# Optimization experiments

Measured on AMD Instinct MI355X. Metric: run time of the kernel, lower is better.

Reference implementation:

```python
import jax, jax.numpy as jnp
import numpy as np

EMB = 256
HEADS = 4
HEAD_DIM = EMB // HEADS
N = 4096
M = 4096


def setup_inputs() -> dict:
    key = jax.random.key(0)
    ks = jax.random.split(key, 7)
    s = 1.0 / np.sqrt(EMB)  # keep logits in a sane range
    return {
        "A": jax.random.normal(ks[0], (N, EMB), jnp.float32),
        "B": jax.random.normal(ks[1], (M, EMB), jnp.float32),
        "Wq": jax.random.normal(ks[2], (EMB, EMB), jnp.float32) * s,
        "Wk": jax.random.normal(ks[3], (EMB, EMB), jnp.float32) * s,
        "Wv": jax.random.normal(ks[4], (EMB, EMB), jnp.float32) * s,
        "Wo": jax.random.normal(ks[5], (EMB, EMB), jnp.float32) * s,
        "bo": jnp.zeros((EMB,), jnp.float32),
    }


def _cross_attend(X, Y, Wq, Wk, Wv, Wo, bo):
    # X attends to Y. X:[n,emb], Y:[m,emb]
    scale = jnp.asarray(np.sqrt(HEAD_DIM), X.dtype)
    Q = (X @ Wq.T).reshape(X.shape[0], HEADS, HEAD_DIM)  # [n,h,d]
    K = (Y @ Wk.T).reshape(Y.shape[0], HEADS, HEAD_DIM)  # [m,h,d]
    V = (Y @ Wv.T).reshape(Y.shape[0], HEADS, HEAD_DIM)  # [m,h,d]
    scores = jnp.einsum("nhd,mhd->hnm", Q, K) / scale      # [h,n,m]
    attn = jax.nn.softmax(scores, axis=-1)                   # dropout p=0.0 -> identity
    ctx = jnp.einsum("hnm,mhd->nhd", attn, V).reshape(X.shape[0], EMB)
    return ctx @ Wo.T + bo + X                               # out proj + residual


def reference(A, B, Wq, Wk, Wv, Wo, bo):
    A_out = _cross_attend(A, B, Wq, Wk, Wv, Wo, bo)
    B_out = _cross_attend(B, A, Wq, Wk, Wv, Wo, bo)
    return (A_out, B_out)
```

## Files before the change

### kernel.cpp

```cpp
#include <hip/hip_runtime.h>
#include <hip/hip_bf16.h>
#include <math.h>

#define EMB 256
#define HEADS 4
#define HD 64
#define NTOK 4096

typedef __attribute__((ext_vector_type(8))) short bf16x8;
typedef __attribute__((ext_vector_type(4))) float f32x4;
typedef __attribute__((ext_vector_type(16))) float f32x16;

#define MFMA16(a, b, c) __builtin_amdgcn_mfma_f32_16x16x32_bf16(a, b, c, 0, 0, 0)
#define MFMA32(a, b, c) __builtin_amdgcn_mfma_f32_32x32x16_bf16(a, b, c, 0, 0, 0)

static __device__ __forceinline__ ushort f2bf(float f) {
    __hip_bfloat16 h = __float2bfloat16(f);
    return *(ushort*)&h;
}
static __device__ __forceinline__ float ex2(float x) { return __builtin_amdgcn_exp2f(x); }
static __device__ __forceinline__ uint pkbf(float lo, float hi) {
    uint r;
    asm("v_cvt_pk_bf16_f32 %0, %1, %2" : "=v"(r) : "v"(lo), "v"(hi));
    return r;
}
static __device__ __forceinline__ float max3f(float a, float b, float c) {
    float r;
    asm("v_max3_f32 %0, %1, %2, %3" : "=v"(r) : "v"(a), "v"(b), "v"(c));
    return r;
}
static __device__ __forceinline__ bf16x8 cvt8(float4 a, float4 b) {
    union { uint u[4]; bf16x8 h; } pk;
    pk.u[0] = pkbf(a.x, a.y);
    pk.u[1] = pkbf(a.z, a.w);
    pk.u[2] = pkbf(b.x, b.y);
    pk.u[3] = pkbf(b.z, b.w);
    return pk.h;
}
static __device__ __forceinline__ float bf2f(ushort u) {
    return __uint_as_float(((uint)u) << 16);
}

__global__ void cvtW(const float* __restrict__ Wq, const float* __restrict__ Wk,
                     const float* __restrict__ Wv, const float* __restrict__ Wo,
                     ushort* __restrict__ Wall) {
    const float* s = (blockIdx.y == 0) ? Wq : (blockIdx.y == 1) ? Wk : (blockIdx.y == 2) ? Wv : Wo;
    ushort* d = Wall + (size_t)blockIdx.y * 65536;
    int i = (blockIdx.x * 256 + threadIdx.x) * 4;
    float4 v = *(const float4*)(s + i);
    ushort4 o;
    o.x = f2bf(v.x); o.y = f2bf(v.y); o.z = f2bf(v.z); o.w = f2bf(v.w);
    *(ushort4*)(d + i) = o;
}

__global__ __launch_bounds__(256) void qkv_proj(const float* __restrict__ Xa,
                                                const float* __restrict__ Xb,
                                                const ushort* __restrict__ Wall,
                                                ushort* __restrict__ Q0, ushort* __restrict__ K1, ushort* __restrict__ Vt1,
                                                ushort* __restrict__ Q1, ushort* __restrict__ K0, ushort* __restrict__ Vt0) {
    int w = threadIdx.x >> 6, lane = threadIdx.x & 63;
    int lr = lane & 15, lg = lane >> 4;
    int z = blockIdx.z;
    int kind = (z < 3) ? z : z - 3;
    const float* X = (z < 3) ? Xa : Xb;
    ushort* Qo = (z < 3) ? Q0 : Q1;
    ushort* Ko = (z < 3) ? K1 : K0;
    ushort* Vto = (z < 3) ? Vt1 : Vt0;
    const ushort* W = Wall + (size_t)kind * 65536;
    int rbase = blockIdx.x * 64 + w * 16;
    int cbase = blockIdx.y * 64;

    f32x4 acc[4] = {};
#pragma unroll
    for (int kk = 0; kk < 256; kk += 32) {
        const float* xr = X + (size_t)(rbase + lr) * EMB + kk + lg * 8;
        bf16x8 a = cvt8(*(const float4*)xr, *(const float4*)(xr + 4));
#pragma unroll
        for (int cj = 0; cj < 4; ++cj) {
            bf16x8 b = *(const bf16x8*)(W + (size_t)(cbase + cj * 16 + lr) * EMB + kk + lg * 8);
            acc[cj] = MFMA16(a, b, acc[cj]);
        }
    }
    const float QS = 0.125f * 1.4426950408889634f;
#pragma unroll
    for (int cj = 0; cj < 4; ++cj)
#pragma unroll
        for (int j = 0; j < 4; ++j) {
            int R = rbase + lg * 4 + j;
            int col = cbase + cj * 16 + lr;
            float v = acc[cj][j];
            if (kind == 0) {
                Qo[(size_t)R * EMB + col] = f2bf(v * QS);
            } else if (kind == 1) {
                Ko[(size_t)R * EMB + col] = f2bf(v);
            } else {
                int h = col >> 6, d = col & 63;
                int Rp = (R & ~12) | ((R & 4) << 1) | ((R & 8) >> 1);
                Vto[(size_t)h * HD * NTOK + (size_t)d * NTOK + Rp] = f2bf(v);
            }
        }
}

__global__ __launch_bounds__(256, 4) void attn(const ushort* __restrict__ Q0,
                                               const ushort* __restrict__ K0,
                                               const ushort* __restrict__ Vt0,
                                               const ushort* __restrict__ Q1,
                                               const ushort* __restrict__ K1,
                                               const ushort* __restrict__ Vt1,
                                               ushort* __restrict__ Opart,
                                               float* __restrict__ ML) {
    __shared__ ushort lK[2][64 * 64];
    __shared__ ushort lV[2][64 * 64];

    int fb = blockIdx.x + 32 * blockIdx.y + 128 * blockIdx.z;
    int nf = (fb & 7) * 128 + (fb >> 3);
    int qt = nf & 31;
    int head = (nf >> 5) & 3;
    int z = nf >> 7;
    int dir = z >> 2, split = z & 3;
    int kv0 = split * 1024;

    const ushort* Q = dir ? Q1 : Q0;
    const ushort* K = dir ? K1 : K0;
    const ushort* Vt = dir ? Vt1 : Vt0;
    const ushort* Vth = Vt + (size_t)head * HD * NTOK;

    int wq = threadIdx.x >> 6;
    int lane = threadIdx.x & 63;
    int l31 = lane & 31, hi = lane >> 5;

    int qg = qt * 128 + wq * 32 + l31;
    bf16x8 qf[4];
#pragma unroll
    for (int ks = 0; ks < 4; ++ks)
        qf[ks] = *(const bf16x8*)(Q + (size_t)qg * EMB + head * 64 + ks * 16 + hi * 8);

    int srow = threadIdx.x >> 3, sseg = threadIdx.x & 7;
    int ssw0 = (sseg ^ (srow & 7)) * 8;
    int ssw1 = (sseg ^ ((srow + 32) & 7)) * 8;

    uint4 rk0 = *(const uint4*)(K + (size_t)(kv0 + srow) * EMB + head * 64 + sseg * 8);
    uint4 rk1 = *(const uint4*)(K + (size_t)(kv0 + srow + 32) * EMB + head * 64 + sseg * 8);
    uint4 rv0 = *(const uint4*)(Vth + (size_t)srow * NTOK + kv0 + sseg * 8);
    uint4 rv1 = *(const uint4*)(Vth + (size_t)(srow + 32) * NTOK + kv0 + sseg * 8);

    float m = -1e30f, ls = 0.0f;
    f32x16 oacc0 = {};
    f32x16 oacc1 = {};
    int sw = l31 & 7;

    for (int t = 0; t < 16; ++t) {
        int cur = t & 1;
        ushort* lk = &lK[cur][0];
        ushort* lv = &lV[cur][0];
        *(uint4*)(&lk[srow * 64 + ssw0]) = rk0;
        *(uint4*)(&lk[(srow + 32) * 64 + ssw1]) = rk1;
        *(uint4*)(&lv[srow * 64 + ssw0]) = rv0;
        *(uint4*)(&lv[(srow + 32) * 64 + ssw1]) = rv1;
        __syncthreads();

        if (t < 15) {
            int nkv = kv0 + (t + 1) * 64;
            rk0 = *(const uint4*)(K + (size_t)(nkv + srow) * EMB + head * 64 + sseg * 8);
            rk1 = *(const uint4*)(K + (size_t)(nkv + srow + 32) * EMB + head * 64 + sseg * 8);
            rv0 = *(const uint4*)(Vth + (size_t)srow * NTOK + nkv + sseg * 8);
            rv1 = *(const uint4*)(Vth + (size_t)(srow + 32) * NTOK + nkv + sseg * 8);
        }

        f32x16 sA = {}, sB = {};
        __builtin_amdgcn_s_setprio(1);
#pragma unroll
        for (int ks = 0; ks < 4; ++ks) {
            bf16x8 ka = *(const bf16x8*)(&lk[l31 * 64 + ((ks * 2 + hi) ^ sw) * 8]);
            bf16x8 kb = *(const bf16x8*)(&lk[(32 + l31) * 64 + ((ks * 2 + hi) ^ sw) * 8]);
            sA = MFMA32(ka, qf[ks], sA);
            sB = MFMA32(kb, qf[ks], sB);
        }
        __builtin_amdgcn_s_setprio(0);

        float t0 = max3f(sA[0], sA[1], sA[2]);
        float t1 = max3f(sA[3], sA[4], sA[5]);
        float t2 = max3f(sA[6], sA[7], sA[8]);
        float t3 = max3f(sA[9], sA[10], sA[11]);
        float t4 = max3f(sA[12], sA[13], sA[14]);
        float t5 = max3f(sB[0], sB[1], sB[2]);
        float t6 = max3f(sB[3], sB[4], sB[5]);
        float t7 = max3f(sB[6], sB[7], sB[8]);
        float t8 = max3f(sB[9], sB[10], sB[11]);
        float t9 = max3f(sB[12], sB[13], sB[14]);
        float ta = fmaxf(sA[15], sB[15]);
        float u0 = max3f(t0, t1, t2);
        float u1 = max3f(t3, t4, t5);
        float u2 = max3f(t6, t7, t8);
        float u3 = fmaxf(t9, ta);
        float tmax = fmaxf(max3f(u0, u1, u2), u3);
        tmax = fmaxf(tmax, __shfl_xor(tmax, 32));

        if (__any(tmax > m + 8.0f)) {
            float mn = fmaxf(m, tmax);
            float sc = ex2(m - mn);
            m = mn;
            ls *= sc;
#pragma unroll
            for (int r = 0; r < 16; ++r) { oacc0[r] *= sc; oacc1[r] *= sc; }
        }

#pragma unroll
        for (int r = 0; r < 16; ++r) sA[r] = ex2(sA[r] - m);
#pragma unroll
        for (int r = 0; r < 16; ++r) sB[r] = ex2(sB[r] - m);

        float s1[16];
#pragma unroll
        for (int i = 0; i < 8; ++i) s1[i] = sA[2 * i] + sA[2 * i + 1];
#pragma unroll
        for (int i = 0; i < 8; ++i) s1[8 + i] = sB[2 * i] + sB[2 * i + 1];
#pragma unroll
        for (int w2 = 8; w2 >= 1; w2 >>= 1)
#pragma unroll
            for (int i = 0; i < 8; ++i)
                if (i < w2) s1[i] = s1[2 * i] + s1[2 * i + 1];
        float rs = s1[0];
        rs += __shfl_xor(rs, 32);
        ls += rs;

        bf16x8 pa[4];
#pragma unroll
        for (int ks = 0; ks < 4; ++ks) {
            union { uint u[4]; bf16x8 h; } pk;
#pragma unroll
            for (int j = 0; j < 4; ++j) {
                float lo = (ks < 2) ? sA[(ks & 1) * 8 + 2 * j] : sB[(ks & 1) * 8 + 2 * j];
                float hv = (ks < 2) ? sA[(ks & 1) * 8 + 2 * j + 1] : sB[(ks & 1) * 8 + 2 * j + 1];
                pk.u[j] = pkbf(lo, hv);
            }
            pa[ks] = pk.h;
        }

        __builtin_amdgcn_s_setprio(1);
#pragma unroll
        for (int ks = 0; ks < 4; ++ks) {
            bf16x8 va = *(const bf16x8*)(&lv[l31 * 64 + ((ks * 2 + hi) ^ sw) * 8]);
            bf16x8 vb = *(const bf16x8*)(&lv[(32 + l31) * 64 + ((ks * 2 + hi) ^ sw) * 8]);
            oacc0 = MFMA32(va, pa[ks], oacc0);
            oacc1 = MFMA32(vb, pa[ks], oacc1);
        }
        __builtin_amdgcn_s_setprio(0);
    }

    ushort* Ob = Opart + ((size_t)z * 4096 + qg) * 256 + head * 64;
#pragma unroll
    for (int r = 0; r < 16; ++r) {
        int crow = (r & 3) + 8 * (r >> 2) + 4 * hi;
        Ob[crow] = f2bf(oacc0[r]);
        Ob[32 + crow] = f2bf(oacc1[r]);
    }
    if (hi == 0) {
        float2* mlp = (float2*)ML;
        mlp[((size_t)z * 4 + head) * 4096 + qg] = make_float2(m, ls);
    }
}

__global__ __launch_bounds__(256) void out_proj(const ushort* __restrict__ Opart,
                                                const float* __restrict__ ML,
                                                const ushort* __restrict__ Wo,
                                                const float* __restrict__ bo,
                                                const float* __restrict__ A,
                                                const float* __restrict__ B,
                                                float* __restrict__ out) {
    int dir = blockIdx.z;
    const float* X = dir ? B : A;
    float* o = out + (size_t)dir * NTOK * EMB;

    int w = threadIdx.x >> 6, lane = threadIdx.x & 63;
    int lr = lane & 15, lg = lane >> 4;
    int rbase = blockIdx.x * 64 + w * 16;
    int cbase = blockIdx.y * 64;
    int R = rbase + lr;

    const float2* mlp = (const float2*)ML;
    float Wm[4][4];
#pragma unroll
    for (int h = 0; h < 4; ++h) {
        float2 ml[4];
        float M = -1e30f;
#pragma unroll
        for (int s = 0; s < 4; ++s) {
            ml[s] = mlp[((size_t)(dir * 4 + s) * 4 + h) * 4096 + R];
            M = fmaxf(M, ml[s].x);
        }
        float denom = 0.0f, a[4];
#pragma unroll
        for (int s = 0; s < 4; ++s) { a[s] = ex2(ml[s].x - M); denom += a[s] * ml[s].y; }
        float inv = 1.0f / denom;
#pragma unroll
        for (int s = 0; s < 4; ++s) Wm[h][s] = a[s] * inv;
    }

    const ushort* Or[4];
#pragma unroll
    for (int s = 0; s < 4; ++s)
        Or[s] = Opart + ((size_t)(dir * 4 + s) * 4096 + R) * 256;

    f32x4 acc[4] = {};
#pragma unroll
    for (int kk = 0; kk < 256; kk += 32) {
        int h = kk >> 6;
        bf16x8 xs0 = *(const bf16x8*)(Or[0] + kk + lg * 8);
        bf16x8 xs1 = *(const bf16x8*)(Or[1] + kk + lg * 8);
        bf16x8 xs2 = *(const bf16x8*)(Or[2] + kk + lg * 8);
        bf16x8 xs3 = *(const bf16x8*)(Or[3] + kk + lg * 8);
        float cv[8];
#pragma unroll
        for (int u = 0; u < 8; ++u) {
            cv[u] = Wm[h][0] * bf2f((ushort)xs0[u]) + Wm[h][1] * bf2f((ushort)xs1[u])
                  + Wm[h][2] * bf2f((ushort)xs2[u]) + Wm[h][3] * bf2f((ushort)xs3[u]);
        }
        float4 c0 = {cv[0], cv[1], cv[2], cv[3]};
        float4 c1 = {cv[4], cv[5], cv[6], cv[7]};
        bf16x8 a = cvt8(c0, c1);
#pragma unroll
        for (int cj = 0; cj < 4; ++cj) {
            bf16x8 b = *(const bf16x8*)(Wo + (size_t)(cbase + cj * 16 + lr) * EMB + kk + lg * 8);
            acc[cj] = MFMA16(a, b, acc[cj]);
        }
    }
#pragma unroll
    for (int cj = 0; cj < 4; ++cj)
#pragma unroll
        for (int j = 0; j < 4; ++j) {
            int Rr = rbase + lg * 4 + j;
            int col = cbase + cj * 16 + lr;
            o[(size_t)Rr * EMB + col] = acc[cj][j] + bo[col] + X[(size_t)Rr * EMB + col];
        }
}

extern "C" void kernel_launch(void* const* d_in, const int* in_sizes, int n_in,
                              void* d_out, int out_size, void* d_ws, size_t ws_size,
                              hipStream_t stream) {
    const float* A  = (const float*)d_in[0];
    const float* B  = (const float*)d_in[1];
    const float* Wq = (const float*)d_in[2];
    const float* Wk = (const float*)d_in[3];
    const float* Wv = (const float*)d_in[4];
    const float* Wo = (const float*)d_in[5];
    const float* bo = (const float*)d_in[6];
    float* out = (float*)d_out;

    ushort* ws = (ushort*)d_ws;
    const size_t TE = (size_t)NTOK * EMB;
    ushort* wall = ws;
    ushort* q0  = wall + 4 * 65536;
    ushort* q1  = q0 + TE;
    ushort* k0  = q1 + TE;
    ushort* k1  = k0 + TE;
    ushort* vt0 = k1 + TE;
    ushort* vt1 = vt0 + TE;
    ushort* Opart = vt1 + TE;
    float* ML = (float*)(Opart + (size_t)8 * 4096 * 256);

    cvtW<<<dim3(64, 4), 256, 0, stream>>>(Wq, Wk, Wv, Wo, wall);

    qkv_proj<<<dim3(64, 4, 6), 256, 0, stream>>>(A, B, wall, q0, k1, vt1, q1, k0, vt0);

    attn<<<dim3(32, 4, 8), 256, 0, stream>>>(q0, k0, vt0, q1, k1, vt1, Opart, ML);

    out_proj<<<dim3(64, 4, 2), 256, 0, stream>>>(Opart, ML, wall + 3 * 65536, bo, A, B, out);
}
```

Baseline: 113.8 us.

## Single-buffer K/V in LDS, change swizzle, use permlane32 swap for reductions

Result: no change. 113.4 us (-0.4%).

```diff
diff --git a/kernel.cpp b/kernel.cpp
--- a/kernel.cpp
+++ b/kernel.cpp
@@ -10,6 +10,7 @@
 typedef __attribute__((ext_vector_type(8))) short bf16x8;
 typedef __attribute__((ext_vector_type(4))) float f32x4;
 typedef __attribute__((ext_vector_type(16))) float f32x16;
+typedef __attribute__((ext_vector_type(2))) unsigned int uint2v;
 
 #define MFMA16(a, b, c) __builtin_amdgcn_mfma_f32_16x16x32_bf16(a, b, c, 0, 0, 0)
 #define MFMA32(a, b, c) __builtin_amdgcn_mfma_f32_32x32x16_bf16(a, b, c, 0, 0, 0)
@@ -28,6 +29,16 @@
     float r;
     asm("v_max3_f32 %0, %1, %2, %3" : "=v"(r) : "v"(a), "v"(b), "v"(c));
     return r;
+}
+static __device__ __forceinline__ float redmax32(float x) {
+    uint xi = __float_as_uint(x);
+    uint2v r = __builtin_amdgcn_permlane32_swap(xi, xi, false, false);
+    return fmaxf(__uint_as_float(r[0]), __uint_as_float(r[1]));
+}
+static __device__ __forceinline__ float redsum32(float x) {
+    uint xi = __float_as_uint(x);
+    uint2v r = __builtin_amdgcn_permlane32_swap(xi, xi, false, false);
+    return __uint_as_float(r[0]) + __uint_as_float(r[1]);
 }
 static __device__ __forceinline__ bf16x8 cvt8(float4 a, float4 b) {
     union { uint u[4]; bf16x8 h; } pk;
@@ -109,8 +120,8 @@
                                                const ushort* __restrict__ Vt1,
                                                ushort* __restrict__ Opart,
                                                float* __restrict__ ML) {
-    __shared__ ushort lK[2][64 * 64];
-    __shared__ ushort lV[2][64 * 64];
+    __shared__ ushort lK[64 * 64];
+    __shared__ ushort lV[64 * 64];
 
     int fb = blockIdx.x + 32 * blockIdx.y + 128 * blockIdx.z;
     int nf = (fb & 7) * 128 + (fb >> 3);
@@ -136,8 +147,7 @@
         qf[ks] = *(const bf16x8*)(Q + (size_t)qg * EMB + head * 64 + ks * 16 + hi * 8);
 
     int srow = threadIdx.x >> 3, sseg = threadIdx.x & 7;
-    int ssw0 = (sseg ^ (srow & 7)) * 8;
-    int ssw1 = (sseg ^ ((srow + 32) & 7)) * 8;
+    int ssw = (sseg ^ ((srow >> 2) & 7)) * 8;
 
     uint4 rk0 = *(const uint4*)(K + (size_t)(kv0 + srow) * EMB + head * 64 + sseg * 8);
     uint4 rk1 = *(const uint4*)(K + (size_t)(kv0 + srow + 32) * EMB + head * 64 + sseg * 8);
@@ -147,16 +157,14 @@
     float m = -1e30f, ls = 0.0f;
     f32x16 oacc0 = {};
     f32x16 oacc1 = {};
-    int sw = l31 & 7;
+    int sw = (l31 >> 2) & 7;
 
     for (int t = 0; t < 16; ++t) {
-        int cur = t & 1;
-        ushort* lk = &lK[cur][0];
-        ushort* lv = &lV[cur][0];
-        *(uint4*)(&lk[srow * 64 + ssw0]) = rk0;
-        *(uint4*)(&lk[(srow + 32) * 64 + ssw1]) = rk1;
-        *(uint4*)(&lv[srow * 64 + ssw0]) = rv0;
-        *(uint4*)(&lv[(srow + 32) * 64 + ssw1]) = rv1;
+        if (t) __syncthreads();
+        *(uint4*)(&lK[srow * 64 + ssw]) = rk0;
+        *(uint4*)(&lK[(srow + 32) * 64 + ssw]) = rk1;
+        *(uint4*)(&lV[srow * 64 + ssw]) = rv0;
+        *(uint4*)(&lV[(srow + 32) * 64 + ssw]) = rv1;
         __syncthreads();
 
         if (t < 15) {
@@ -171,8 +179,8 @@
         __builtin_amdgcn_s_setprio(1);
 #pragma unroll
         for (int ks = 0; ks < 4; ++ks) {
-            bf16x8 ka = *(const bf16x8*)(&lk[l31 * 64 + ((ks * 2 + hi) ^ sw) * 8]);
-            bf16x8 kb = *(const bf16x8*)(&lk[(32 + l31) * 64 + ((ks * 2 + hi) ^ sw) * 8]);
+            bf16x8 ka = *(const bf16x8*)(&lK[l31 * 64 + ((ks * 2 + hi) ^ sw) * 8]);
+            bf16x8 kb = *(const bf16x8*)(&lK[(32 + l31) * 64 + ((ks * 2 + hi) ^ sw) * 8]);
             sA = MFMA32(ka, qf[ks], sA);
             sB = MFMA32(kb, qf[ks], sB);
         }
@@ -193,8 +201,7 @@
         float u1 = max3f(t3, t4, t5);
         float u2 = max3f(t6, t7, t8);
         float u3 = fmaxf(t9, ta);
-        float tmax = fmaxf(max3f(u0, u1, u2), u3);
-        tmax = fmaxf(tmax, __shfl_xor(tmax, 32));
+        float tmax = redmax32(fmaxf(max3f(u0, u1, u2), u3));
 
         if (__any(tmax > m + 8.0f)) {
             float mn = fmaxf(m, tmax);
@@ -220,9 +227,7 @@
 #pragma unroll
             for (int i = 0; i < 8; ++i)
                 if (i < w2) s1[i] = s1[2 * i] + s1[2 * i + 1];
-        float rs = s1[0];
-        rs += __shfl_xor(rs, 32);
-        ls += rs;
+        ls += redsum32(s1[0]);
 
         bf16x8 pa[4];
 #pragma unroll
@@ -240,8 +245,8 @@
         __builtin_amdgcn_s_setprio(1);
 #pragma unroll
         for (int ks = 0; ks < 4; ++ks) {
-            bf16x8 va = *(const bf16x8*)(&lv[l31 * 64 + ((ks * 2 + hi) ^ sw) * 8]);
-            bf16x8 vb = *(const bf16x8*)(&lv[(32 + l31) * 64 + ((ks * 2 + hi) ^ sw) * 8]);
+            bf16x8 va = *(const bf16x8*)(&lV[l31 * 64 + ((ks * 2 + hi) ^ sw) * 8]);
+            bf16x8 vb = *(const bf16x8*)(&lV[(32 + l31) * 64 + ((ks * 2 + hi) ^ sw) * 8]);
             oacc0 = MFMA32(va, pa[ks], oacc0);
             oacc1 = MFMA32(vb, pa[ks], oacc1);
         }
```
